# Performance work log

Hardware: AMD Instinct MI355X
Metric: run time of the kernel (lower is better)

The kernel has to match this reference:

```python
import jax, jax.numpy as jnp
import numpy as np

N = 30000      # num nodes (cells)
E = 480000     # num edges (avg degree 16)
D_IN = 1000    # input_dim (genes)
H = 8          # nheads
F_H = 32       # hidden_dim per head
D_EMB = 64     # embedding_dim
NEG_SLOPE = 0.2


def setup_inputs() -> dict:
    key = jax.random.key(0)
    ks = jax.random.split(key, 12)
    glorot = lambda k, shape, fan: (jax.random.normal(k, shape, jnp.float32)
                                    * (1.0 / np.sqrt(fan)))
    return {
        "x": jax.random.normal(ks[0], (N, D_IN), jnp.float32),
        "edge_index": jax.random.randint(ks[1], (2, E), 0, N),
        "edge_weight": jax.random.uniform(ks[2], (E,), jnp.float32),
        # GATConv params
        "W": glorot(ks[3], (D_IN, H * F_H), D_IN),
        "att_src": glorot(ks[4], (H, F_H), F_H),
        "att_dst": glorot(ks[5], (H, F_H), F_H),
        "bias_gat": jnp.zeros((H * F_H,), jnp.float32),
        # embedding Linear
        "emb_W": glorot(ks[6], (H * F_H, D_EMB), H * F_H),
        "emb_b": jnp.zeros((D_EMB,), jnp.float32),
        # decoder MLP
        "dec_W1": glorot(ks[7], (D_EMB, F_H), D_EMB),
        "dec_b1": jnp.zeros((F_H,), jnp.float32),
        "dec_W2": glorot(ks[8], (F_H, D_IN), F_H),
        "dec_b2": jnp.zeros((D_IN,), jnp.float32),
    }


def _gat_conv(x, edge_index, W, att_src, att_dst, bias):
    n = x.shape[0]
    h = (x @ W).reshape(n, H, F_H)                    # [N,H,F]
    a_s = jnp.einsum('nhf,hf->nh', h, att_src)        # [N,H]
    a_d = jnp.einsum('nhf,hf->nh', h, att_dst)        # [N,H]
    # add self loops (PyG default add_self_loops=True)
    loops = jnp.arange(n)
    src = jnp.concatenate([edge_index[0], loops])     # [E+N]
    dst = jnp.concatenate([edge_index[1], loops])     # [E+N]
    logits = jax.nn.leaky_relu(a_s[src] + a_d[dst], NEG_SLOPE)  # [E+N,H]
    # segment softmax over incoming edges of each destination node
    m = jax.ops.segment_max(logits, dst, num_segments=n)        # [N,H]
    p = jnp.exp(logits - m[dst])
    denom = jax.ops.segment_sum(p, dst, num_segments=n)         # [N,H]
    alpha = p / denom[dst]                                      # [E+N,H]
    msg = h[src] * alpha[:, :, None]                            # [E+N,H,F]
    out = jax.ops.segment_sum(msg, dst, num_segments=n)         # [N,H,F]
    return out.reshape(n, H * F_H) + bias


def reference(x, edge_index, edge_weight, W, att_src, att_dst, bias_gat,
              emb_W, emb_b, dec_W1, dec_b1, dec_W2, dec_b2):
    # edge_weight is accepted but unused: PyG GATConv with edge_dim=None has
    # no edge-feature pathway.
    h = jax.nn.relu(_gat_conv(x, edge_index, W, att_src, att_dst, bias_gat))
    z = h @ emb_W + emb_b                               # [N, D_EMB]
    d = jax.nn.relu(z @ dec_W1 + dec_b1)                # [N, F_H]
    recon = d @ dec_W2 + dec_b2                         # [N, D_IN]
    return recon, z
```

## Files before the change

kernel.cpp:

```cpp
#include <hip/hip_runtime.h>
#include <hip/hip_bf16.h>

#define N_NODES 30000
#define N_EDGES 480000
#define D_IN    1000
#define KPAD    1024
#define NHEAD   8
#define F_HID   32
#define D_EMB   64
#define NEG_SLOPE 0.2f
#define MAXDEG  64

typedef __attribute__((ext_vector_type(4))) float  f32x4;
typedef __attribute__((ext_vector_type(8))) __bf16 bf16x8;
typedef __attribute__((ext_vector_type(4))) __bf16 bf16x4;

#define WT_TOT    (256*KPAD + D_EMB*256 + F_HID*D_EMB + D_IN*F_HID)
#define WT_BLOCKS ((WT_TOT + 255) / 256)
#define WA_BLOCKS (16 * KPAD / 256)
#define ZC_BLOCKS ((N_NODES + 255) / 256)

__global__ __launch_bounds__(256) void cvt_w(
    const float* __restrict__ W, const float* __restrict__ emb_W,
    const float* __restrict__ d1, const float* __restrict__ d2,
    const float* __restrict__ att_src, const float* __restrict__ att_dst,
    __bf16* __restrict__ WbT, __bf16* __restrict__ embT,
    __bf16* __restrict__ d1T, __bf16* __restrict__ d2T,
    __bf16* __restrict__ WaT, int* __restrict__ cnt)
{
    int b = blockIdx.x;
    if (b < WT_BLOCKS) {
        int i = b * 256 + threadIdx.x;
        if (i < 256 * KPAD) {
            int n = i >> 10, k = i & 1023;
            WbT[i] = (k < D_IN) ? (__bf16)W[(size_t)k * 256 + n] : (__bf16)0.0f;
            return;
        }
        i -= 256 * KPAD;
        if (i < D_EMB * 256) {
            int n = i >> 8, k = i & 255;
            embT[i] = (__bf16)emb_W[(size_t)k * D_EMB + n];
            return;
        }
        i -= D_EMB * 256;
        if (i < F_HID * D_EMB) {
            int n = i >> 6, k = i & 63;
            d1T[i] = (__bf16)d1[(size_t)k * F_HID + n];
            return;
        }
        i -= F_HID * D_EMB;
        if (i < D_IN * F_HID) {
            int n = i >> 5, k = i & 31;
            d2T[i] = (__bf16)d2[(size_t)k * D_IN + n];
        }
        return;
    }
    b -= WT_BLOCKS;
    if (b < WA_BLOCKS) {
        int i = b * 256 + threadIdx.x;
        int j = i >> 10, k = i & 1023;
        float s = 0.f;
        if (k < D_IN) {
            const float* av = (j < 8 ? att_src : att_dst) + (j & 7) * F_HID;
            const float* wr = W + (size_t)k * 256 + (j & 7) * F_HID;
            #pragma unroll
            for (int f = 0; f < F_HID; f++) s += wr[f] * av[f];
        }
        WaT[i] = (__bf16)s;
        return;
    }
    b -= WA_BLOCKS;
    {
        int i = b * 256 + threadIdx.x;
        if (i < N_NODES) cnt[i] = 0;
    }
}

__device__ __forceinline__ void stage_tile(
    __bf16* lds, const __bf16* __restrict__ g, int base, int maxr,
    int K, int k0, int rows, int w, int lane, int stride)
{
    const int rsub = lane >> 2;
    const int c    = lane & 3;
    for (int off = w * 1024; off < rows * 64; off += stride) {
        int r  = (off >> 6) + rsub;
        int gr = base + r; gr = gr > maxr ? maxr : gr;
        int chunk = c ^ (r & 3);
        const __bf16* gp = g + (size_t)gr * K + k0 + chunk * 8;
        __builtin_amdgcn_global_load_lds(
            (const __attribute__((address_space(1))) void*)gp,
            (__attribute__((address_space(3))) void*)((char*)lds + off),
            16, 0, 0);
    }
}

#define GEMM1_BLOCKS ((N_NODES + 63) / 64)
#define SC512        ((N_EDGES + 511) / 512)

__device__ __forceinline__ void xload8(const float* __restrict__ xrow, int cb,
                                       f32x4& u0, f32x4& u1)
{
    if (cb < D_IN) {
        const f32x4* p = (const f32x4*)(xrow + cb);
        u0 = p[0]; u1 = p[1];
    } else {
        u0 = (f32x4){0.f, 0.f, 0.f, 0.f};
        u1 = (f32x4){0.f, 0.f, 0.f, 0.f};
    }
}

__device__ __forceinline__ bf16x8 cvt8(const f32x4& u0, const f32x4& u1)
{
    bf16x8 o;
    o[0] = (__bf16)u0.x; o[1] = (__bf16)u0.y; o[2] = (__bf16)u0.z; o[3] = (__bf16)u0.w;
    o[4] = (__bf16)u1.x; o[5] = (__bf16)u1.y; o[6] = (__bf16)u1.z; o[7] = (__bf16)u1.w;
    return o;
}

__global__ __launch_bounds__(512, 4) void gemm1_fused(
    const float* __restrict__ x, const __bf16* __restrict__ WbT,
    const __bf16* __restrict__ WaT, __bf16* __restrict__ hb,
    float* __restrict__ a_s, float* __restrict__ a_d,
    const int* __restrict__ eidx, int* __restrict__ cnt,
    int* __restrict__ slots, int M)
{
    __shared__ __align__(16) __bf16 As[2][64 * 32];
    __shared__ __align__(16) __bf16 Bs[2][256 * 32];

    if (blockIdx.x >= GEMM1_BLOCKS) {
        int e = (blockIdx.x - GEMM1_BLOCKS) * 512 + threadIdx.x;
        if (e < N_EDGES) {
            int d = eidx[N_EDGES + e];
            int slot = atomicAdd(&cnt[d], 1);
            slots[d * MAXDEG + slot] = eidx[e];
        }
        return;
    }

    const int tid  = threadIdx.x;
    const int w    = tid >> 6, lane = tid & 63;
    const int wm   = w >> 2,   wn   = w & 3;
    const int quad = lane >> 4, l16 = lane & 15;
    const int bm   = blockIdx.x * 64;

    const bool astage = (tid < 256);
    const int r0   = tid >> 2;
    const int cpos = tid & 3;
    const int cxor = (cpos ^ (r0 & 3)) << 3;
    int grow = bm + r0; if (grow > M - 1) grow = M - 1;
    const float* xrow = x + (size_t)grow * D_IN;

    const int brsub = lane >> 2;
    const int bc    = lane & 3;

    f32x4 acc[2][4];
    #pragma unroll
    for (int i = 0; i < 2; i++)
        #pragma unroll
        for (int j = 0; j < 4; j++)
            acc[i][j] = (f32x4){0.f, 0.f, 0.f, 0.f};
    f32x4 accA[2];
    #pragma unroll
    for (int i = 0; i < 2; i++) accA[i] = (f32x4){0.f, 0.f, 0.f, 0.f};

    const bool att = (wn == 0);
    const __bf16* warow = WaT + (size_t)l16 * KPAD + quad * 8;

    auto stageB = [&](int buf, int k0) {
        #pragma unroll
        for (int off = 0; off < 16384; off += 8192) {
            int o2 = off + w * 1024;
            int r = (o2 >> 6) + brsub;
            int chunk = bc ^ (r & 3);
            const __bf16* gp = WbT + (size_t)r * KPAD + k0 + chunk * 8;
            __builtin_amdgcn_global_load_lds(
                (const __attribute__((address_space(1))) void*)gp,
                (__attribute__((address_space(3))) void*)((char*)&Bs[buf][0] + o2),
                16, 0, 0);
        }
    };

    auto compute = [&](int buf, const bf16x8& attfrag) {
        bf16x8 af[2], bfr[4];
        #pragma unroll
        for (int mt = 0; mt < 2; mt++) {
            int r = wm * 32 + mt * 16 + l16;
            af[mt] = *(const bf16x8*)&As[buf][r * 32 + (quad ^ (r & 3)) * 8];
        }
        #pragma unroll
        for (int nt = 0; nt < 4; nt++) {
            int r = wn * 64 + nt * 16 + l16;
            bfr[nt] = *(const bf16x8*)&Bs[buf][r * 32 + (quad ^ (r & 3)) * 8];
        }
        #pragma unroll
        for (int mt = 0; mt < 2; mt++)
            #pragma unroll
            for (int nt = 0; nt < 4; nt++)
                acc[mt][nt] = __builtin_amdgcn_mfma_f32_16x16x32_bf16(
                    af[mt], bfr[nt], acc[mt][nt], 0, 0, 0);
        if (att) {
            #pragma unroll
            for (int mt = 0; mt < 2; mt++)
                accA[mt] = __builtin_amdgcn_mfma_f32_16x16x32_bf16(
                    af[mt], attfrag, accA[mt], 0, 0, 0);
        }
    };

    f32x4 xa0, xa1, xb0, xb1;
    bf16x8 attEv = {}, attOd = {};

    if (astage) {
        xload8(xrow, 0 + cxor, xa0, xa1);
        xload8(xrow, 32 + cxor, xb0, xb1);
    }
    if (att) attEv = *(const bf16x8*)(warow + 0);
    if (astage) *(bf16x8*)&As[0][r0 * 32 + cpos * 8] = cvt8(xa0, xa1);
    stageB(0, 0);
    __syncthreads();

    for (int k0 = 0; k0 < KPAD; k0 += 64) {
        if (astage) {
            xload8(xrow, (k0 + 64) + cxor, xa0, xa1);
            *(bf16x8*)&As[1][r0 * 32 + cpos * 8] = cvt8(xb0, xb1);
        }
        if (att) attOd = *(const bf16x8*)(warow + k0 + 32);
        stageB(1, k0 + 32);
        compute(0, attEv);
        __syncthreads();

        if (k0 + 64 < KPAD) {
            if (astage) {
                xload8(xrow, (k0 + 96) + cxor, xb0, xb1);
                *(bf16x8*)&As[0][r0 * 32 + cpos * 8] = cvt8(xa0, xa1);
            }
            if (att) attEv = *(const bf16x8*)(warow + k0 + 64);
            stageB(0, k0 + 64);
        }
        compute(1, attOd);
        __syncthreads();
    }

    #pragma unroll
    for (int nt = 0; nt < 4; nt++) {
        int col = wn * 64 + nt * 16 + l16;
        #pragma unroll
        for (int mt = 0; mt < 2; mt++) {
            int row0 = bm + wm * 32 + mt * 16 + quad * 4;
            #pragma unroll
            for (int rr = 0; rr < 4; rr++) {
                int row = row0 + rr;
                if (row < M)
                    hb[(size_t)row * 256 + col] = (__bf16)acc[mt][nt][rr];
            }
        }
    }
    if (att) {
        #pragma unroll
        for (int mt = 0; mt < 2; mt++) {
            int row0 = bm + wm * 32 + mt * 16 + quad * 4;
            #pragma unroll
            for (int rr = 0; rr < 4; rr++) {
                int row = row0 + rr;
                if (row < M) {
                    float v = accA[mt][rr];
                    if (l16 < 8) a_s[row * NHEAD + l16] = v;
                    else         a_d[row * NHEAD + (l16 - 8)] = v;
                }
            }
        }
    }
}

__device__ __forceinline__ float leaky(float x) {
    return x > 0.f ? x : NEG_SLOPE * x;
}

__global__ __launch_bounds__(256) void gat_aggregate(
    const __bf16* __restrict__ hb, const float* __restrict__ a_s,
    const float* __restrict__ a_d, const int* __restrict__ cnt,
    const int* __restrict__ slots, const float* __restrict__ bias,
    __bf16* __restrict__ hgatb)
{
    const int wid  = threadIdx.x >> 6;
    const int lane = threadIdx.x & 63;
    const int n = blockIdx.x * 4 + wid;
    if (n >= N_NODES) return;

    const int hh = lane >> 3;
    const int fo = (lane & 7) * 4;
    const int base = n * MAXDEG;
    const int c = cnt[n];
    const float adn = a_d[n * NHEAD + hh];

    float p = __expf(leaky(a_s[n * NHEAD + hh] + adn));
    float denom = p;
    f32x4 acc;
    {
        bf16x4 hv = *(const bf16x4*)(hb + (size_t)n * 256 + hh * F_HID + fo);
        acc.x = p * (float)hv[0]; acc.y = p * (float)hv[1];
        acc.z = p * (float)hv[2]; acc.w = p * (float)hv[3];
    }
    int e = 0;
    for (; e + 4 <= c; e += 4) {
        const int4 ss = *(const int4*)(slots + base + e);
        int s0 = ss.x, s1 = ss.y, s2 = ss.z, s3 = ss.w;
        float l0 = a_s[s0 * NHEAD + hh], l1 = a_s[s1 * NHEAD + hh];
        float l2 = a_s[s2 * NHEAD + hh], l3 = a_s[s3 * NHEAD + hh];
        bf16x4 h0 = *(const bf16x4*)(hb + (size_t)s0 * 256 + hh * F_HID + fo);
        bf16x4 h1 = *(const bf16x4*)(hb + (size_t)s1 * 256 + hh * F_HID + fo);
        bf16x4 h2 = *(const bf16x4*)(hb + (size_t)s2 * 256 + hh * F_HID + fo);
        bf16x4 h3 = *(const bf16x4*)(hb + (size_t)s3 * 256 + hh * F_HID + fo);
        float p0 = __expf(leaky(l0 + adn)), p1 = __expf(leaky(l1 + adn));
        float p2 = __expf(leaky(l2 + adn)), p3 = __expf(leaky(l3 + adn));
        denom += (p0 + p1) + (p2 + p3);
        acc.x += p0*(float)h0[0] + p1*(float)h1[0] + p2*(float)h2[0] + p3*(float)h3[0];
        acc.y += p0*(float)h0[1] + p1*(float)h1[1] + p2*(float)h2[1] + p3*(float)h3[1];
        acc.z += p0*(float)h0[2] + p1*(float)h1[2] + p2*(float)h2[2] + p3*(float)h3[2];
        acc.w += p0*(float)h0[3] + p1*(float)h1[3] + p2*(float)h2[3] + p3*(float)h3[3];
    }
    for (; e < c; e++) {
        int s = slots[base + e];
        float pe = __expf(leaky(a_s[s * NHEAD + hh] + adn));
        denom += pe;
        bf16x4 hv = *(const bf16x4*)(hb + (size_t)s * 256 + hh * F_HID + fo);
        acc.x += pe * (float)hv[0]; acc.y += pe * (float)hv[1];
        acc.z += pe * (float)hv[2]; acc.w += pe * (float)hv[3];
    }
    float inv = 1.0f / denom;
    f32x4 bv = *(const f32x4*)(bias + lane * 4);
    float o0 = acc.x * inv + bv.x, o1 = acc.y * inv + bv.y;
    float o2 = acc.z * inv + bv.z, o3 = acc.w * inv + bv.w;
    o0 = o0 > 0.f ? o0 : 0.f;
    o1 = o1 > 0.f ? o1 : 0.f;
    o2 = o2 > 0.f ? o2 : 0.f;
    o3 = o3 > 0.f ? o3 : 0.f;
    bf16x4 ob;
    ob[0] = (__bf16)o0; ob[1] = (__bf16)o1; ob[2] = (__bf16)o2; ob[3] = (__bf16)o3;
    *(bf16x4*)(hgatb + (size_t)n * 256 + lane * 4) = ob;
}

__global__ __launch_bounds__(256) void gemm_zdr(
    const __bf16* __restrict__ hgatb, const __bf16* __restrict__ embT,
    const __bf16* __restrict__ d1T, const __bf16* __restrict__ d2T,
    const float* __restrict__ emb_b, const float* __restrict__ dec_b1,
    const float* __restrict__ dec_b2, float* __restrict__ z,
    float* __restrict__ recon, int M)
{
    __shared__ __align__(16) __bf16 smem[16384];
    __bf16* As  = smem;
    __bf16* Bs  = smem + 4096;
    __bf16* zS  = smem + 6144;
    __bf16* Bs2 = smem + 14336;

    const int tid  = threadIdx.x;
    const int w    = tid >> 6, lane = tid & 63;
    const int wm   = w >> 1,   wn   = w & 1;
    const int quad = lane >> 4, l16 = lane & 15;
    const int bm = blockIdx.x * 128;

    stage_tile(Bs2,        d1T, 0, 31, 64, 0,  32, w, lane, 4096);
    stage_tile(Bs2 + 1024, d1T, 0, 31, 64, 32, 32, w, lane, 4096);

    f32x4 acc[4][2];
    #pragma unroll
    for (int i = 0; i < 4; i++) { acc[i][0] = (f32x4){0,0,0,0}; acc[i][1] = (f32x4){0,0,0,0}; }

    for (int k0 = 0; k0 < 256; k0 += 32) {
        stage_tile(As, hgatb, bm, M - 1, 256, k0, 128, w, lane, 4096);
        stage_tile(Bs, embT,  0,  D_EMB - 1, 256, k0, 64, w, lane, 4096);
        __syncthreads();
        bf16x8 af[4], bfr[2];
        #pragma unroll
        for (int mt = 0; mt < 4; mt++) {
            int r = wm * 64 + mt * 16 + l16;
            af[mt] = *(const bf16x8*)&As[r * 32 + (quad ^ (r & 3)) * 8];
        }
        #pragma unroll
        for (int nt = 0; nt < 2; nt++) {
            int r = wn * 32 + nt * 16 + l16;
            bfr[nt] = *(const bf16x8*)&Bs[r * 32 + (quad ^ (r & 3)) * 8];
        }
        #pragma unroll
        for (int mt = 0; mt < 4; mt++)
            #pragma unroll
            for (int nt = 0; nt < 2; nt++)
                acc[mt][nt] = __builtin_amdgcn_mfma_f32_16x16x32_bf16(
                    af[mt], bfr[nt], acc[mt][nt], 0, 0, 0);
        __syncthreads();
    }

    #pragma unroll
    for (int nt = 0; nt < 2; nt++) {
        int col = wn * 32 + nt * 16 + l16;
        float bv = emb_b[col];
        int t = col >> 5, cch = (col >> 3) & 3, j = col & 7;
        #pragma unroll
        for (int mt = 0; mt < 4; mt++) {
            int rl0 = wm * 64 + mt * 16 + quad * 4;
            #pragma unroll
            for (int rr = 0; rr < 4; rr++) {
                int rl = rl0 + rr;
                int row = bm + rl;
                float v = acc[mt][nt][rr] + bv;
                if (row < M) z[(size_t)row * D_EMB + col] = v;
                zS[t * 4096 + rl * 32 + (cch ^ (rl & 3)) * 8 + j] = (__bf16)v;
            }
        }
    }
    __syncthreads();

    f32x4 accd[4];
    #pragma unroll
    for (int i = 0; i < 4; i++) accd[i] = (f32x4){0,0,0,0};
    #pragma unroll
    for (int t = 0; t < 2; t++) {
        bf16x8 af[4], bfr;
        #pragma unroll
        for (int mt = 0; mt < 4; mt++) {
            int r = wm * 64 + mt * 16 + l16;
            af[mt] = *(const bf16x8*)&zS[t * 4096 + r * 32 + (quad ^ (r & 3)) * 8];
        }
        {
            int r = wn * 16 + l16;
            bfr = *(const bf16x8*)&Bs2[t * 1024 + r * 32 + (quad ^ (r & 3)) * 8];
        }
        #pragma unroll
        for (int mt = 0; mt < 4; mt++)
            accd[mt] = __builtin_amdgcn_mfma_f32_16x16x32_bf16(af[mt], bfr, accd[mt], 0, 0, 0);
    }
    {
        int col = wn * 16 + l16;
        float bv = dec_b1[col];
        int cc = col >> 3, j = col & 7;
        #pragma unroll
        for (int mt = 0; mt < 4; mt++) {
            int rl0 = wm * 64 + mt * 16 + quad * 4;
            #pragma unroll
            for (int rr = 0; rr < 4; rr++) {
                int rl = rl0 + rr;
                float v = accd[mt][rr] + bv;
                v = v > 0.f ? v : 0.f;
                As[rl * 32 + (cc ^ (rl & 3)) * 8 + j] = (__bf16)v;
            }
        }
    }
    __syncthreads();

    bf16x8 daf[4];
    #pragma unroll
    for (int mt = 0; mt < 4; mt++) {
        int r = wm * 64 + mt * 16 + l16;
        daf[mt] = *(const bf16x8*)&As[r * 32 + (quad ^ (r & 3)) * 8];
    }
    for (int tt = wn; tt < 63; tt += 2) {
        int col = tt * 16 + l16;
        int crow = col < D_IN ? col : D_IN - 1;
        bf16x8 bfr = *(const bf16x8*)&d2T[(size_t)crow * 32 + quad * 8];
        f32x4 a[4];
        #pragma unroll
        for (int mt = 0; mt < 4; mt++) {
            a[mt] = (f32x4){0.f, 0.f, 0.f, 0.f};
            a[mt] = __builtin_amdgcn_mfma_f32_16x16x32_bf16(daf[mt], bfr, a[mt], 0, 0, 0);
        }
        if (col < D_IN) {
            float bv = dec_b2[col];
            #pragma unroll
            for (int mt = 0; mt < 4; mt++) {
                int row0 = bm + wm * 64 + mt * 16 + quad * 4;
                #pragma unroll
                for (int rr = 0; rr < 4; rr++) {
                    int row = row0 + rr;
                    if (row < M)
                        recon[(size_t)row * D_IN + col] = a[mt][rr] + bv;
                }
            }
        }
    }
}

extern "C" void kernel_launch(void* const* d_in, const int* in_sizes, int n_in,
                              void* d_out, int out_size, void* d_ws, size_t ws_size,
                              hipStream_t stream)
{
    const float* x        = (const float*)d_in[0];
    const int*   eidx     = (const int*)  d_in[1];
    const float* W        = (const float*)d_in[3];
    const float* att_src  = (const float*)d_in[4];
    const float* att_dst  = (const float*)d_in[5];
    const float* bias_gat = (const float*)d_in[6];
    const float* emb_W    = (const float*)d_in[7];
    const float* emb_b    = (const float*)d_in[8];
    const float* dec_W1   = (const float*)d_in[9];
    const float* dec_b1   = (const float*)d_in[10];
    const float* dec_W2   = (const float*)d_in[11];
    const float* dec_b2   = (const float*)d_in[12];

    float* out   = (float*)d_out;
    float* recon = out;
    float* z     = out + (size_t)N_NODES * D_IN;

    char* ws = (char*)d_ws;
    size_t o = 0;
    auto alloc = [&](size_t bytes) { char* p = ws + o; o = (o + bytes + 255) & ~(size_t)255; return p; };
    __bf16* hb      = (__bf16*)alloc((size_t)N_NODES * 256 * 2);
    __bf16* WbT     = (__bf16*)alloc((size_t)256 * KPAD * 2);
    __bf16* embT    = (__bf16*)alloc((size_t)D_EMB * 256 * 2);
    __bf16* d1T     = (__bf16*)alloc((size_t)F_HID * D_EMB * 2);
    __bf16* d2T     = (__bf16*)alloc((size_t)D_IN * F_HID * 2);
    __bf16* WaT     = (__bf16*)alloc((size_t)16 * KPAD * 2);
    __bf16* hgatb   = (__bf16*)alloc((size_t)N_NODES * 256 * 2);
    float*  a_s     = (float*) alloc((size_t)N_NODES * NHEAD * 4);
    float*  a_d     = (float*) alloc((size_t)N_NODES * NHEAD * 4);
    int*    slots   = (int*)   alloc((size_t)N_NODES * MAXDEG * 4);
    int*    cnt     = (int*)   alloc((size_t)N_NODES * 4);

    cvt_w<<<WT_BLOCKS + WA_BLOCKS + ZC_BLOCKS, 256, 0, stream>>>(
        W, emb_W, dec_W1, dec_W2, att_src, att_dst,
        WbT, embT, d1T, d2T, WaT, cnt);

    gemm1_fused<<<GEMM1_BLOCKS + SC512, 512, 0, stream>>>(
        x, WbT, WaT, hb, a_s, a_d, eidx, cnt, slots, N_NODES);

    gat_aggregate<<<N_NODES / 4, 256, 0, stream>>>(
        hb, a_s, a_d, cnt, slots, bias_gat, hgatb);

    gemm_zdr<<<(N_NODES + 127) / 128, 256, 0, stream>>>(
        hgatb, embT, d1T, d2T, emb_b, dec_b1, dec_b2, z, recon, N_NODES);
}
```

Before: 394.7 us.

## Move edge scatter into weight-convert kernel with sharded destination ownership

The edge bucketing scatter (atomicAdd on per-node counts plus slot writes) moves out of the GEMM1 launch into the weight-conversion kernel. Each edge chunk is scanned by 8 blocks, and each block handles only destinations whose bits 4-6 match its shard index, aiming for better atomic and write locality per block. The count zeroing becomes a hipMemsetAsync before the kernel. In exchange every edge's destination is read 8 times, the scatter no longer overlaps with the GEMM, and an extra memset call is added.

```diff
diff --git a/kernel.cpp b/kernel.cpp
--- a/kernel.cpp
+++ b/kernel.cpp
@@ -18,7 +18,8 @@
 #define WT_TOT    (256*KPAD + D_EMB*256 + F_HID*D_EMB + D_IN*F_HID)
 #define WT_BLOCKS ((WT_TOT + 255) / 256)
 #define WA_BLOCKS (16 * KPAD / 256)
-#define ZC_BLOCKS ((N_NODES + 255) / 256)
+#define SC_CHUNK  4068
+#define SC_BLOCKS (118 * 8)
 
 __global__ __launch_bounds__(256) void cvt_w(
     const float* __restrict__ W, const float* __restrict__ emb_W,
@@ -26,7 +27,9 @@
     const float* __restrict__ att_src, const float* __restrict__ att_dst,
     __bf16* __restrict__ WbT, __bf16* __restrict__ embT,
     __bf16* __restrict__ d1T, __bf16* __restrict__ d2T,
-    __bf16* __restrict__ WaT, int* __restrict__ cnt)
+    __bf16* __restrict__ WaT,
+    const int* __restrict__ eidx, int* __restrict__ cnt,
+    int* __restrict__ slots)
 {
     int b = blockIdx.x;
     if (b < WT_BLOCKS) {
@@ -71,8 +74,17 @@
     }
     b -= WA_BLOCKS;
     {
-        int i = b * 256 + threadIdx.x;
-        if (i < N_NODES) cnt[i] = 0;
+        const int shard = blockIdx.x & 7;
+        const int chunk = b >> 3;
+        int e0 = chunk * SC_CHUNK;
+        int e1 = e0 + SC_CHUNK; if (e1 > N_EDGES) e1 = N_EDGES;
+        for (int e = e0 + (int)threadIdx.x; e < e1; e += 256) {
+            int d = eidx[N_EDGES + e];
+            if (((d >> 4) & 7) == shard) {
+                int slot = atomicAdd(&cnt[d], 1);
+                slots[d * MAXDEG + slot] = eidx[e];
+            }
+        }
     }
 }
 
@@ -95,7 +107,6 @@
 }
 
 #define GEMM1_BLOCKS ((N_NODES + 63) / 64)
-#define SC512        ((N_EDGES + 511) / 512)
 
 __device__ __forceinline__ void xload8(const float* __restrict__ xrow, int cb,
                                        f32x4& u0, f32x4& u1)
@@ -120,22 +131,10 @@
 __global__ __launch_bounds__(512, 4) void gemm1_fused(
     const float* __restrict__ x, const __bf16* __restrict__ WbT,
     const __bf16* __restrict__ WaT, __bf16* __restrict__ hb,
-    float* __restrict__ a_s, float* __restrict__ a_d,
-    const int* __restrict__ eidx, int* __restrict__ cnt,
-    int* __restrict__ slots, int M)
+    float* __restrict__ a_s, float* __restrict__ a_d, int M)
 {
     __shared__ __align__(16) __bf16 As[2][64 * 32];
     __shared__ __align__(16) __bf16 Bs[2][256 * 32];
-
-    if (blockIdx.x >= GEMM1_BLOCKS) {
-        int e = (blockIdx.x - GEMM1_BLOCKS) * 512 + threadIdx.x;
-        if (e < N_EDGES) {
-            int d = eidx[N_EDGES + e];
-            int slot = atomicAdd(&cnt[d], 1);
-            slots[d * MAXDEG + slot] = eidx[e];
-        }
-        return;
-    }
 
     const int tid  = threadIdx.x;
     const int w    = tid >> 6, lane = tid & 63;
@@ -514,12 +513,14 @@
     int*    slots   = (int*)   alloc((size_t)N_NODES * MAXDEG * 4);
     int*    cnt     = (int*)   alloc((size_t)N_NODES * 4);
 
-    cvt_w<<<WT_BLOCKS + WA_BLOCKS + ZC_BLOCKS, 256, 0, stream>>>(
+    hipMemsetAsync(cnt, 0, (size_t)N_NODES * 4, stream);
+
+    cvt_w<<<WT_BLOCKS + WA_BLOCKS + SC_BLOCKS, 256, 0, stream>>>(
         W, emb_W, dec_W1, dec_W2, att_src, att_dst,
-        WbT, embT, d1T, d2T, WaT, cnt);
-
-    gemm1_fused<<<GEMM1_BLOCKS + SC512, 512, 0, stream>>>(
-        x, WbT, WaT, hb, a_s, a_d, eidx, cnt, slots, N_NODES);
+        WbT, embT, d1T, d2T, WaT, eidx, cnt, slots);
+
+    gemm1_fused<<<GEMM1_BLOCKS, 512, 0, stream>>>(
+        x, WbT, WaT, hb, a_s, a_d, N_NODES);
 
     gat_aggregate<<<N_NODES / 4, 256, 0, stream>>>(
         hb, a_s, a_d, cnt, slots, bias_gat, hgatb);
```

Measured after the change: 398.0 us. About the same (+0.8%).
